# Kernel tuning notes

Measured on AMD Instinct MI355X. Metric: run time of the kernel, lower is better.

Reference implementation:

```python
import jax, jax.numpy as jnp
import numpy as np

OBS, ACT, EMB, DET, STO = 512, 32, 1024, 1024, 256
T, B = 64, 256
KL_SCALE = 1.0


def setup_inputs() -> dict:
    key = jax.random.key(0)
    ks = jax.random.split(key, 24)
    s = 0.02
    inp = {
        "obs": jax.random.normal(ks[0], (T, B, OBS), jnp.float32),
        "actions": jax.random.normal(ks[1], (T, B, ACT), jnp.float32),
        "rewards": jax.random.normal(ks[2], (T, B), jnp.float32),
        "dones": jnp.zeros((T, B), jnp.bool_),
        "eps": jax.random.normal(ks[3], (T - 1, B, STO), jnp.float32),
        # encoder: Linear(OBS,EMB) -> ReLU -> Linear(EMB,EMB) -> ReLU
        "enc_w1": jax.random.normal(ks[4], (OBS, EMB)) * s,
        "enc_b1": jnp.zeros((EMB,)),
        "enc_w2": jax.random.normal(ks[5], (EMB, EMB)) * s,
        "enc_b2": jnp.zeros((EMB,)),
        # GRUCell(STO+ACT, DET), torch layout [3*DET, in], gate order r,z,n
        "gru_wih": jax.random.normal(ks[6], (3 * DET, STO + ACT)) * s,
        "gru_whh": jax.random.normal(ks[7], (3 * DET, DET)) * s,
        "gru_bih": jnp.zeros((3 * DET,)),
        "gru_bhh": jnp.zeros((3 * DET,)),
        # prior / posterior nets
        "prior_w": jax.random.normal(ks[8], (DET, 2 * STO)) * s,
        "prior_b": jnp.zeros((2 * STO,)),
        "post_w": jax.random.normal(ks[9], (DET + EMB, 2 * STO)) * s,
        "post_b": jnp.zeros((2 * STO,)),
        # obs decoder
        "dec_w1": jax.random.normal(ks[10], (DET + STO, EMB)) * s,
        "dec_b1": jnp.zeros((EMB,)),
        "dec_w2": jax.random.normal(ks[11], (EMB, OBS)) * s,
        "dec_b2": jnp.zeros((OBS,)),
        # reward head
        "rew_w1": jax.random.normal(ks[12], (DET + STO, EMB)) * s,
        "rew_b1": jnp.zeros((EMB,)),
        "rew_w2": jax.random.normal(ks[13], (EMB, 1)) * s,
        "rew_b2": jnp.zeros((1,)),
    }
    return inp


def _kl(mq, lq, mp, lp):
    vq = jnp.exp(2.0 * lq)
    vp = jnp.exp(2.0 * lp)
    kl = lp - lq + (vq + (mq - mp) ** 2) / (vp + 1e-8) - 1.0
    return 0.5 * jnp.sum(kl, axis=-1)


def reference(obs, actions, rewards, dones, eps,
              enc_w1, enc_b1, enc_w2, enc_b2,
              gru_wih, gru_whh, gru_bih, gru_bhh,
              prior_w, prior_b, post_w, post_b,
              dec_w1, dec_b1, dec_w2, dec_b2,
              rew_w1, rew_b1, rew_w2, rew_b2):
    def step(carry, xs):
        h, z = carry
        o_t, o_next, a_t, r_t, d_t, e_t = xs
        # encoder
        emb = jax.nn.relu(jax.nn.relu(o_t @ enc_w1 + enc_b1) @ enc_w2 + enc_b2)
        # prior / posterior
        pm, pl = jnp.split(h @ prior_w + prior_b, 2, axis=-1)
        qm, ql = jnp.split(jnp.concatenate([h, emb], -1) @ post_w + post_b, 2, axis=-1)
        z_post = qm + e_t * jnp.exp(ql)
        # GRUCell (torch semantics)
        x = jnp.concatenate([z_post, a_t], -1)
        gi = x @ gru_wih.T + gru_bih
        gh = h @ gru_whh.T + gru_bhh
        ir, iz, inn = jnp.split(gi, 3, -1)
        hr, hz, hn = jnp.split(gh, 3, -1)
        r = jax.nn.sigmoid(ir + hr)
        u = jax.nn.sigmoid(iz + hz)
        n = jnp.tanh(inn + r * hn)
        h_next = (1.0 - u) * n + u * h
        feat = jnp.concatenate([h_next, z_post], -1)
        pred_obs = jax.nn.relu(feat @ dec_w1 + dec_b1) @ dec_w2 + dec_b2
        pred_rew = (jax.nn.relu(feat @ rew_w1 + rew_b1) @ rew_w2 + rew_b2)[..., 0]
        recon = jnp.mean((pred_obs - o_next) ** 2, axis=-1)  # [B]
        rew_l = (pred_rew - r_t) ** 2                         # [B]
        kl = _kl(qm, ql, pm, pl)                              # [B]
        mask = 1.0 - d_t.astype(h_next.dtype)[:, None]
        return (h_next * mask, z_post * mask), (recon, rew_l, kl)

    h0 = jnp.zeros((B, DET), obs.dtype)
    z0 = jnp.zeros((B, STO), obs.dtype)
    xs = (obs[:-1], obs[1:], actions[:-1], rewards[:-1], dones[:-1], eps)
    _, (recon, rew_l, kl) = jax.lax.scan(step, (h0, z0), xs)
    recon_loss = jnp.mean(recon)
    reward_loss = jnp.mean(rew_l)
    kl_loss = jnp.mean(kl)
    total = recon_loss + reward_loss + KL_SCALE * kl_loss
    return jnp.stack([total, recon_loss, reward_loss, kl_loss])
```

## Files before the change

### kernel.cpp

```cpp
#include <hip/hip_runtime.h>
#include <math.h>


namespace {

typedef unsigned short ushort;
typedef __attribute__((ext_vector_type(8))) short short8;
typedef __attribute__((ext_vector_type(4))) float f32x4;

constexpr int TSTEPS = 63;
constexpr int NB     = 256;
constexpr int NACT   = 32;
constexpr int NROWS  = TSTEPS * NB;
constexpr int TGRP   = 7;
constexpr int NGRP   = 9;
constexpr int GROWS  = TGRP * NB;

constexpr size_t OFF_POSTE = 0;
constexpr size_t OFF_OBSB  = OFF_POSTE + (size_t)NROWS * 512;
constexpr size_t OFF_E1C   = OFF_OBSB + (size_t)GROWS * 512 / 2;
constexpr size_t OFF_EMBC  = OFF_E1C + (size_t)GROWS * 1024 / 2;
constexpr size_t OFF_FEATC = OFF_EMBC + (size_t)GROWS * 1024 / 2;
constexpr size_t OFF_DR1C  = OFF_FEATC + (size_t)GROWS * 1280 / 2;
constexpr size_t OFF_WHT   = OFF_DR1C + (size_t)GROWS * 2048 / 2;
constexpr size_t OFF_WIHT  = OFF_WHT + (size_t)4096 * 1024 / 2;
constexpr size_t OFF_WDRT  = OFF_WIHT + (size_t)3072 * 288 / 2;
constexpr size_t OFF_E1T   = OFF_WDRT + (size_t)2048 * 1280 / 2;
constexpr size_t OFF_E2T   = OFF_E1T + (size_t)1024 * 512 / 2;
constexpr size_t OFF_PET   = OFF_E2T + (size_t)1024 * 1024 / 2;
constexpr size_t OFF_DW2T  = OFF_PET + (size_t)512 * 1024 / 2;
constexpr size_t OFF_BDR   = OFF_DW2T + (size_t)512 * 1024 / 2;
constexpr size_t OFF_G     = OFF_BDR + 2048;
constexpr size_t OFF_H     = OFF_G + (size_t)NB * 3072;
constexpr size_t OFF_HB    = OFF_H + (size_t)NB * 1024;
constexpr size_t OFF_ACC   = OFF_HB + (size_t)NB * 1024 / 2;
constexpr size_t OFF_XBUF  = OFF_ACC + 16;

__device__ __forceinline__ ushort f2bf(float f) {
  unsigned int u = __float_as_uint(f);
  unsigned int r = (u + 0x7fffu + ((u >> 16) & 1u)) >> 16;
  return (ushort)r;
}
__device__ __forceinline__ float bf2f(ushort u) {
  return __uint_as_float((unsigned int)u << 16);
}

__global__ void zero_kernel(float* p, int n) {
  int i = blockIdx.x * 256 + threadIdx.x;
  if (i < n) p[i] = 0.f;
}

__global__ void f2bf_kernel(const float* __restrict__ in, ushort* __restrict__ out, int n) {
  int i = blockIdx.x * 256 + threadIdx.x;
  if (i < n) out[i] = f2bf(in[i]);
}

__global__ void build_wht(const float* __restrict__ prior_w, const float* __restrict__ post_w,
                          const float* __restrict__ whh, ushort* __restrict__ out) {
  int idx = blockIdx.x * 256 + threadIdx.x;
  int n = idx >> 10, k = idx & 1023;
  float v;
  if (n < 1024) {
    int q = (n >> 4) & 3;
    int s = ((n >> 6) << 4) | (n & 15);
    v = (q == 0) ? prior_w[k * 512 + s]
      : (q == 1) ? prior_w[k * 512 + 256 + s]
      : (q == 2) ? post_w[k * 512 + s]
                 : post_w[k * 512 + 256 + s];
  } else {
    v = whh[(size_t)(n - 1024) * 1024 + k];
  }
  out[idx] = f2bf(v);
}

__global__ void trans_conv(const float* __restrict__ in, ushort* __restrict__ out,
                           int ldi, int ldo) {
  __shared__ float tile[32][33];
  int r0 = blockIdx.y * 32, c0 = blockIdx.x * 32;
  int tx = threadIdx.x & 31, ty = threadIdx.x >> 5;
#pragma unroll
  for (int p = 0; p < 4; ++p)
    tile[ty + p * 8][tx] = in[(size_t)(r0 + ty + p * 8) * ldi + c0 + tx];
  __syncthreads();
#pragma unroll
  for (int p = 0; p < 4; ++p)
    out[(size_t)(c0 + ty + p * 8) * ldo + r0 + tx] = f2bf(tile[tx][ty + p * 8]);
}

__global__ void build_bdr(const float* __restrict__ dec_b1, const float* __restrict__ rew_b1,
                          float* __restrict__ bdr) {
  int i = blockIdx.x * 256 + threadIdx.x;
  bdr[i] = (i < 1024) ? dec_b1[i] : rew_b1[i - 1024];
}

template <int EPI>
__global__ __launch_bounds__(256) void gemm_bf16(
    const ushort* __restrict__ A, const ushort* __restrict__ BT,
    const float* __restrict__ bias, void* __restrict__ Cv,
    int K, int lda, int ldb, int ldc) {
  __shared__ __align__(16) ushort As[64 * 40];
  __shared__ __align__(16) ushort Bs[64 * 40];
  int tid = threadIdx.x;
  int wave = tid >> 6, lane = tid & 63;
  int quad = lane >> 4, l15 = lane & 15;
  int m0 = blockIdx.y * 64, n0 = blockIdx.x * 64;
  int sr = tid >> 2, sc = (tid & 3) * 8;
  f32x4 acc[4] = {};
  for (int k0 = 0; k0 < K; k0 += 32) {
    *(int4*)&As[sr * 40 + sc] = *(const int4*)(A + (size_t)(m0 + sr) * lda + k0 + sc);
    *(int4*)&Bs[sr * 40 + sc] = *(const int4*)(BT + (size_t)(n0 + sr) * ldb + k0 + sc);
    __syncthreads();
    short8 a = *(const short8*)&As[(wave * 16 + l15) * 40 + quad * 8];
#pragma unroll
    for (int c = 0; c < 4; ++c) {
      short8 b = *(const short8*)&Bs[(c * 16 + l15) * 40 + quad * 8];
      acc[c] = __builtin_amdgcn_mfma_f32_16x16x32_bf16(a, b, acc[c], 0, 0, 0);
    }
    __syncthreads();
  }
#pragma unroll
  for (int c = 0; c < 4; ++c) {
#pragma unroll
    for (int r = 0; r < 4; ++r) {
      size_t row = m0 + wave * 16 + quad * 4 + r;
      int col = n0 + c * 16 + l15;
      float v = acc[c][r] + bias[col];
      if (EPI == 1) v = fmaxf(v, 0.f);
      if (EPI == 1) ((ushort*)Cv)[row * ldc + col] = f2bf(v);
      else ((float*)Cv)[row * ldc + col] = v;
    }
  }
}

__global__ __launch_bounds__(256) void step_g_kernel(
    int t, int tt, const ushort* __restrict__ HB, const ushort* __restrict__ WHT,
    const float* __restrict__ prior_b, const float* __restrict__ poste,
    const float* __restrict__ eps, const float* __restrict__ actions,
    float* __restrict__ G, ushort* __restrict__ xbuf,
    ushort* __restrict__ featc, float* __restrict__ acc_kl) {
  __shared__ __align__(16) ushort As[64 * 72];
  __shared__ __align__(16) ushort Bs[64 * 72];
  int tid = threadIdx.x;
  int wave = tid >> 6, lane = tid & 63;
  int quad = lane >> 4, l15 = lane & 15;
  int m0 = blockIdx.y * 64, n0 = blockIdx.x * 64;
  int sr = tid >> 2, sc = (tid & 3) * 16;
  const ushort* agp = HB + (size_t)(m0 + sr) * 1024 + sc;
  const ushort* bgp = WHT + (size_t)(n0 + sr) * 1024 + sc;
  int4 a0 = *(const int4*)agp, a1 = *(const int4*)(agp + 8);
  int4 b0 = *(const int4*)bgp, b1 = *(const int4*)(bgp + 8);
  f32x4 acc[4] = {};
  for (int k0 = 0;;) {
    *(int4*)&As[sr * 72 + sc] = a0; *(int4*)&As[sr * 72 + sc + 8] = a1;
    *(int4*)&Bs[sr * 72 + sc] = b0; *(int4*)&Bs[sr * 72 + sc + 8] = b1;
    __syncthreads();
    int kn = k0 + 64;
    if (kn < 1024) {
      a0 = *(const int4*)(agp + kn); a1 = *(const int4*)(agp + kn + 8);
      b0 = *(const int4*)(bgp + kn); b1 = *(const int4*)(bgp + kn + 8);
    }
#pragma unroll
    for (int kk = 0; kk < 2; ++kk) {
      short8 a = *(const short8*)&As[(wave * 16 + l15) * 72 + kk * 32 + quad * 8];
#pragma unroll
      for (int c = 0; c < 4; ++c) {
        short8 b = *(const short8*)&Bs[(c * 16 + l15) * 72 + kk * 32 + quad * 8];
        acc[c] = __builtin_amdgcn_mfma_f32_16x16x32_bf16(a, b, acc[c], 0, 0, 0);
      }
    }
    k0 = kn;
    if (k0 >= 1024) break;
    __syncthreads();
  }
  if (blockIdx.x < 16) {
    int s = (n0 >> 2) + l15;
    float kl_sum = 0.f;
#pragma unroll
    for (int r = 0; r < 4; ++r) {
      int b = m0 + wave * 16 + quad * 4 + r;
      size_t row = (size_t)t * NB + b;
      float pm = acc[0][r] + prior_b[s];
      float pl = acc[1][r] + prior_b[256 + s];
      float qm = acc[2][r] + poste[row * 512 + s];
      float ql = acc[3][r] + poste[row * 512 + 256 + s];
      float e = eps[row * 256 + s];
      float z = qm + e * expf(ql);
      xbuf[b * 288 + s] = f2bf(z);
      featc[(size_t)(tt * NB + b) * 1280 + 1024 + s] = f2bf(z);
      if (s < NACT) xbuf[b * 288 + 256 + s] = f2bf(actions[row * NACT + s]);
      float vq = expf(2.f * ql), vp = expf(2.f * pl);
      float dm = qm - pm;
      kl_sum += pl - ql + (vq + dm * dm) / (vp + 1e-8f) - 1.f;
    }
    for (int off = 32; off > 0; off >>= 1) kl_sum += __shfl_down(kl_sum, off);
    if (lane == 0) atomicAdd(acc_kl, 0.5f * kl_sum);
  } else {
    int ng = n0 - 1024;
#pragma unroll
    for (int c = 0; c < 4; ++c)
#pragma unroll
      for (int r = 0; r < 4; ++r) {
        int b = m0 + wave * 16 + quad * 4 + r;
        G[(size_t)b * 3072 + ng + c * 16 + l15] = acc[c][r];
      }
  }
}

__global__ __launch_bounds__(256) void gru_step_kernel(
    int t, int tt, const ushort* __restrict__ xbuf, const ushort* __restrict__ wiht,
    const float* __restrict__ G, const float* __restrict__ bih,
    const float* __restrict__ bhh, const unsigned char* __restrict__ dones,
    float* __restrict__ H, ushort* __restrict__ HB, ushort* __restrict__ featc) {
  __shared__ __align__(16) ushort As[64 * 40];
  __shared__ __align__(16) ushort Bs[3][64 * 40];
  int tid = threadIdx.x;
  int wave = tid >> 6, lane = tid & 63;
  int quad = lane >> 4, l15 = lane & 15;
  int m0 = blockIdx.y * 64, n0 = blockIdx.x * 64;
  int sr = tid >> 2, sc = (tid & 3) * 8;
  const ushort* agp = xbuf + (size_t)(m0 + sr) * 288 + sc;
  const ushort* bgp0 = wiht + (size_t)(n0 + sr) * 288 + sc;
  int4 pa = *(const int4*)agp;
  int4 pb0 = *(const int4*)bgp0;
  int4 pb1 = *(const int4*)(bgp0 + (size_t)1024 * 288);
  int4 pb2 = *(const int4*)(bgp0 + (size_t)2048 * 288);
  f32x4 accv[3][4] = {};
  for (int k0 = 0;;) {
    *(int4*)&As[sr * 40 + sc] = pa;
    *(int4*)&Bs[0][sr * 40 + sc] = pb0;
    *(int4*)&Bs[1][sr * 40 + sc] = pb1;
    *(int4*)&Bs[2][sr * 40 + sc] = pb2;
    __syncthreads();
    int kn = k0 + 32;
    if (kn < 288) {
      pa = *(const int4*)(agp + kn);
      pb0 = *(const int4*)(bgp0 + kn);
      pb1 = *(const int4*)(bgp0 + (size_t)1024 * 288 + kn);
      pb2 = *(const int4*)(bgp0 + (size_t)2048 * 288 + kn);
    }
    short8 a = *(const short8*)&As[(wave * 16 + l15) * 40 + quad * 8];
#pragma unroll
    for (int gg = 0; gg < 3; ++gg) {
#pragma unroll
      for (int c = 0; c < 4; ++c) {
        short8 b = *(const short8*)&Bs[gg][(c * 16 + l15) * 40 + quad * 8];
        accv[gg][c] = __builtin_amdgcn_mfma_f32_16x16x32_bf16(a, b, accv[gg][c], 0, 0, 0);
      }
    }
    k0 = kn;
    if (k0 >= 288) break;
    __syncthreads();
  }
#pragma unroll
  for (int c = 0; c < 4; ++c) {
#pragma unroll
    for (int r = 0; r < 4; ++r) {
      int b_idx = m0 + wave * 16 + quad * 4 + r;
      int j = n0 + c * 16 + l15;
      const float* g = G + (size_t)b_idx * 3072;
      float ir = accv[0][c][r] + bih[j];
      float iz = accv[1][c][r] + bih[1024 + j];
      float in_ = accv[2][c][r] + bih[2048 + j];
      float hr = g[j] + bhh[j];
      float hz = g[1024 + j] + bhh[1024 + j];
      float hn = g[2048 + j] + bhh[2048 + j];
      float rg = 1.f / (1.f + expf(-(ir + hr)));
      float u = 1.f / (1.f + expf(-(iz + hz)));
      float n = tanhf(in_ + rg * hn);
      float hprev = H[b_idx * 1024 + j];
      float hnext = (1.f - u) * n + u * hprev;
      featc[(size_t)(tt * NB + b_idx) * 1280 + j] = f2bf(hnext);
      float mask = 1.f - (float)dones[t * NB + b_idx];
      float hm = hnext * mask;
      H[b_idx * 1024 + j] = hm;
      HB[b_idx * 1024 + j] = f2bf(hm);
    }
  }
}

__global__ __launch_bounds__(256) void decobs_loss_kernel(
    const ushort* __restrict__ A, const ushort* __restrict__ BT,
    const float* __restrict__ bias, const float* __restrict__ obs_next_g,
    float* __restrict__ acc) {
  __shared__ __align__(16) ushort As[64 * 40];
  __shared__ __align__(16) ushort Bs[64 * 40];
  int tid = threadIdx.x;
  int wave = tid >> 6, lane = tid & 63;
  int quad = lane >> 4, l15 = lane & 15;
  int m0 = blockIdx.y * 64, n0 = blockIdx.x * 64;
  int sr = tid >> 2, sc = (tid & 3) * 8;
  f32x4 accm[4] = {};
  for (int k0 = 0; k0 < 1024; k0 += 32) {
    *(int4*)&As[sr * 40 + sc] = *(const int4*)(A + (size_t)(m0 + sr) * 2048 + k0 + sc);
    *(int4*)&Bs[sr * 40 + sc] = *(const int4*)(BT + (size_t)(n0 + sr) * 1024 + k0 + sc);
    __syncthreads();
    short8 a = *(const short8*)&As[(wave * 16 + l15) * 40 + quad * 8];
#pragma unroll
    for (int c = 0; c < 4; ++c) {
      short8 b = *(const short8*)&Bs[(c * 16 + l15) * 40 + quad * 8];
      accm[c] = __builtin_amdgcn_mfma_f32_16x16x32_bf16(a, b, accm[c], 0, 0, 0);
    }
    __syncthreads();
  }
  float local = 0.f;
#pragma unroll
  for (int c = 0; c < 4; ++c) {
#pragma unroll
    for (int r = 0; r < 4; ++r) {
      size_t row = m0 + wave * 16 + quad * 4 + r;
      int col = n0 + c * 16 + l15;
      float v = accm[c][r] + bias[col];
      float d = v - obs_next_g[row * 512 + col];
      local += d * d;
    }
  }
  __shared__ float red[256];
  red[tid] = local;
  __syncthreads();
  for (int st = 128; st > 0; st >>= 1) {
    if (tid < st) red[tid] += red[tid + st];
    __syncthreads();
  }
  if (tid == 0) atomicAdd(&acc[0], red[0]);
}

__global__ __launch_bounds__(256) void rew_loss_kernel(
    const ushort* __restrict__ R1, const float* __restrict__ w2,
    const float* __restrict__ b2, const float* __restrict__ rewards_g,
    float* __restrict__ acc) {
  int wave = threadIdx.x >> 6;
  int lane = threadIdx.x & 63;
  int row = blockIdx.x * 4 + wave;
  const ushort* rp = R1 + (size_t)row * 2048;
  float s = 0.f;
#pragma unroll
  for (int i = 0; i < 16; ++i) s += bf2f(rp[lane + 64 * i]) * w2[lane + 64 * i];
  for (int off = 32; off > 0; off >>= 1) s += __shfl_down(s, off);
  if (lane == 0) {
    float d = s + b2[0] - rewards_g[row];
    atomicAdd(&acc[1], d * d);
  }
}

__global__ void finalize_kernel(const float* __restrict__ acc, float* __restrict__ out) {
  float recon = acc[0] / ((float)NROWS * 512.f);
  float rew = acc[1] / (float)NROWS;
  float kl = acc[2] / (float)NROWS;
  out[0] = recon + rew + kl;
  out[1] = recon;
  out[2] = rew;
  out[3] = kl;
}

}

extern "C" void kernel_launch(void* const* d_in, const int* in_sizes, int n_in,
                              void* d_out, int out_size, void* d_ws, size_t ws_size,
                              hipStream_t stream) {
  const float* obs     = (const float*)d_in[0];
  const float* actions = (const float*)d_in[1];
  const float* rewards = (const float*)d_in[2];
  const unsigned char* dones = (const unsigned char*)d_in[3];
  const float* eps     = (const float*)d_in[4];
  const float* enc_w1  = (const float*)d_in[5];
  const float* enc_b1  = (const float*)d_in[6];
  const float* enc_w2  = (const float*)d_in[7];
  const float* enc_b2  = (const float*)d_in[8];
  const float* gru_wih = (const float*)d_in[9];
  const float* gru_whh = (const float*)d_in[10];
  const float* gru_bih = (const float*)d_in[11];
  const float* gru_bhh = (const float*)d_in[12];
  const float* prior_w = (const float*)d_in[13];
  const float* prior_b = (const float*)d_in[14];
  const float* post_w  = (const float*)d_in[15];
  const float* post_b  = (const float*)d_in[16];
  const float* dec_w1  = (const float*)d_in[17];
  const float* dec_b1  = (const float*)d_in[18];
  const float* dec_w2  = (const float*)d_in[19];
  const float* dec_b2  = (const float*)d_in[20];
  const float* rew_w1  = (const float*)d_in[21];
  const float* rew_b1  = (const float*)d_in[22];
  const float* rew_w2  = (const float*)d_in[23];
  const float* rew_b2  = (const float*)d_in[24];
  float* out = (float*)d_out;
  float* ws = (float*)d_ws;

  float*  POSTE = ws + OFF_POSTE;
  ushort* OBSB  = (ushort*)(ws + OFF_OBSB);
  ushort* E1C   = (ushort*)(ws + OFF_E1C);
  ushort* EMBC  = (ushort*)(ws + OFF_EMBC);
  ushort* FEATC = (ushort*)(ws + OFF_FEATC);
  ushort* DR1C  = (ushort*)(ws + OFF_DR1C);
  ushort* WHT   = (ushort*)(ws + OFF_WHT);
  ushort* WIHT  = (ushort*)(ws + OFF_WIHT);
  ushort* WDRT  = (ushort*)(ws + OFF_WDRT);
  ushort* E1T   = (ushort*)(ws + OFF_E1T);
  ushort* E2T   = (ushort*)(ws + OFF_E2T);
  ushort* PET   = (ushort*)(ws + OFF_PET);
  ushort* DW2T  = (ushort*)(ws + OFF_DW2T);
  float*  BDR   = ws + OFF_BDR;
  float*  G     = ws + OFF_G;
  float*  H     = ws + OFF_H;
  ushort* HB    = (ushort*)(ws + OFF_HB);
  float*  ACC   = ws + OFF_ACC;
  ushort* XBUF  = (ushort*)(ws + OFF_XBUF);

  {
    int nzero = NB * 1024 + NB * 512 + 16;
    zero_kernel<<<(nzero + 255) / 256, 256, 0, stream>>>(H, nzero);
  }
  build_wht<<<4096 * 1024 / 256, 256, 0, stream>>>(prior_w, post_w, gru_whh, WHT);
  f2bf_kernel<<<(3072 * 288) / 256, 256, 0, stream>>>(gru_wih, WIHT, 3072 * 288);
  trans_conv<<<dim3(1024 / 32, 1280 / 32), 256, 0, stream>>>(dec_w1, WDRT, 1024, 1280);
  trans_conv<<<dim3(1024 / 32, 1280 / 32), 256, 0, stream>>>(rew_w1, WDRT + (size_t)1024 * 1280, 1024, 1280);
  trans_conv<<<dim3(1024 / 32, 512 / 32), 256, 0, stream>>>(enc_w1, E1T, 1024, 512);
  trans_conv<<<dim3(1024 / 32, 1024 / 32), 256, 0, stream>>>(enc_w2, E2T, 1024, 1024);
  trans_conv<<<dim3(512 / 32, 1024 / 32), 256, 0, stream>>>(post_w + (size_t)1024 * 512, PET, 512, 1024);
  trans_conv<<<dim3(512 / 32, 1024 / 32), 256, 0, stream>>>(dec_w2, DW2T, 512, 1024);
  build_bdr<<<8, 256, 0, stream>>>(dec_b1, rew_b1, BDR);

  for (int g = 0; g < NGRP; ++g) {
    const float* obs_g = obs + (size_t)g * GROWS * 512;
    f2bf_kernel<<<(GROWS * 512) / 256, 256, 0, stream>>>(obs_g, OBSB, GROWS * 512);
    gemm_bf16<1><<<dim3(16, GROWS / 64), 256, 0, stream>>>(
        OBSB, E1T, enc_b1, E1C, 512, 512, 512, 1024);
    gemm_bf16<1><<<dim3(16, GROWS / 64), 256, 0, stream>>>(
        E1C, E2T, enc_b2, EMBC, 1024, 1024, 1024, 1024);
    gemm_bf16<2><<<dim3(8, GROWS / 64), 256, 0, stream>>>(
        EMBC, PET, post_b, POSTE + (size_t)g * GROWS * 512, 1024, 1024, 1024, 512);
  }

  for (int g = 0; g < NGRP; ++g) {
    for (int tt = 0; tt < TGRP; ++tt) {
      int t = g * TGRP + tt;
      step_g_kernel<<<dim3(64, 4), 256, 0, stream>>>(
          t, tt, HB, WHT, prior_b, POSTE, eps, actions, G, XBUF, FEATC, &ACC[2]);
      gru_step_kernel<<<dim3(16, 4), 256, 0, stream>>>(
          t, tt, XBUF, WIHT, G, gru_bih, gru_bhh, dones, H, HB, FEATC);
    }
    gemm_bf16<1><<<dim3(32, GROWS / 64), 256, 0, stream>>>(
        FEATC, WDRT, BDR, DR1C, 1280, 1280, 1280, 2048);
    decobs_loss_kernel<<<dim3(8, GROWS / 64), 256, 0, stream>>>(
        DR1C, DW2T, dec_b2, obs + ((size_t)g * TGRP + 1) * NB * 512, ACC);
    rew_loss_kernel<<<GROWS / 4, 256, 0, stream>>>(
        DR1C + 1024, rew_w2, rew_b2, rewards + (size_t)g * TGRP * NB, ACC);
  }

  finalize_kernel<<<1, 1, 0, stream>>>(ACC, out);
}
```

Measured before the change: 3.129 ms.

## Double-buffer LDS in GEMM kernels, fuse obs conversion, split GRU step blocks

All GEMM-style kernels now use double-buffered shared memory with register prefetch of the next K tile. This removes the second barrier per K iteration and overlaps global loads with MFMA work. The encoder's first GEMM reads the fp32 observations directly and converts them to bf16 in registers, which drops the separate f2bf pass and its intermediate buffer. The GRU step kernel switches to 128-thread blocks covering 32 rows each, doubling the number of blocks for the small recurrent step. The cost is twice the LDS per block.

Result: faster. 3.044 ms (-2.7%).

```diff
diff --git a/kernel.cpp b/kernel.cpp
--- a/kernel.cpp
+++ b/kernel.cpp
@@ -93,30 +93,54 @@
   bdr[i] = (i < 1024) ? dec_b1[i] : rew_b1[i - 1024];
 }
 
-template <int EPI>
+template <int EPI, bool AF32>
 __global__ __launch_bounds__(256) void gemm_bf16(
-    const ushort* __restrict__ A, const ushort* __restrict__ BT,
+    const void* __restrict__ Av, const ushort* __restrict__ BT,
     const float* __restrict__ bias, void* __restrict__ Cv,
     int K, int lda, int ldb, int ldc) {
-  __shared__ __align__(16) ushort As[64 * 40];
-  __shared__ __align__(16) ushort Bs[64 * 40];
+  __shared__ __align__(16) ushort As[2][64 * 40];
+  __shared__ __align__(16) ushort Bs[2][64 * 40];
   int tid = threadIdx.x;
   int wave = tid >> 6, lane = tid & 63;
   int quad = lane >> 4, l15 = lane & 15;
   int m0 = blockIdx.y * 64, n0 = blockIdx.x * 64;
   int sr = tid >> 2, sc = (tid & 3) * 8;
+  const ushort* agb = (const ushort*)Av + (size_t)(m0 + sr) * lda + sc;
+  const float*  agf = (const float*)Av + (size_t)(m0 + sr) * lda + sc;
+  const ushort* bgp = BT + (size_t)(n0 + sr) * ldb + sc;
+  int4 pa0, pa1, pb;
+  if (AF32) { pa0 = *(const int4*)agf; pa1 = *(const int4*)(agf + 4); }
+  else      { pa0 = *(const int4*)agb; }
+  pb = *(const int4*)bgp;
   f32x4 acc[4] = {};
-  for (int k0 = 0; k0 < K; k0 += 32) {
-    *(int4*)&As[sr * 40 + sc] = *(const int4*)(A + (size_t)(m0 + sr) * lda + k0 + sc);
-    *(int4*)&Bs[sr * 40 + sc] = *(const int4*)(BT + (size_t)(n0 + sr) * ldb + k0 + sc);
+  int buf = 0;
+  for (int k0 = 0; k0 < K; k0 += 32, buf ^= 1) {
+    int4 st;
+    if (AF32) {
+      float f[8];
+      *(int4*)&f[0] = pa0; *(int4*)&f[4] = pa1;
+      ushort u[8];
+#pragma unroll
+      for (int i = 0; i < 8; ++i) u[i] = f2bf(f[i]);
+      st = *(const int4*)u;
+    } else {
+      st = pa0;
+    }
+    *(int4*)&As[buf][sr * 40 + sc] = st;
+    *(int4*)&Bs[buf][sr * 40 + sc] = pb;
     __syncthreads();
-    short8 a = *(const short8*)&As[(wave * 16 + l15) * 40 + quad * 8];
+    int kn = k0 + 32;
+    if (kn < K) {
+      if (AF32) { pa0 = *(const int4*)(agf + kn); pa1 = *(const int4*)(agf + kn + 4); }
+      else      { pa0 = *(const int4*)(agb + kn); }
+      pb = *(const int4*)(bgp + kn);
+    }
+    short8 a = *(const short8*)&As[buf][(wave * 16 + l15) * 40 + quad * 8];
 #pragma unroll
     for (int c = 0; c < 4; ++c) {
-      short8 b = *(const short8*)&Bs[(c * 16 + l15) * 40 + quad * 8];
+      short8 b = *(const short8*)&Bs[buf][(c * 16 + l15) * 40 + quad * 8];
       acc[c] = __builtin_amdgcn_mfma_f32_16x16x32_bf16(a, b, acc[c], 0, 0, 0);
     }
-    __syncthreads();
   }
 #pragma unroll
   for (int c = 0; c < 4; ++c) {
@@ -138,8 +162,8 @@
     const float* __restrict__ eps, const float* __restrict__ actions,
     float* __restrict__ G, ushort* __restrict__ xbuf,
     ushort* __restrict__ featc, float* __restrict__ acc_kl) {
-  __shared__ __align__(16) ushort As[64 * 72];
-  __shared__ __align__(16) ushort Bs[64 * 72];
+  __shared__ __align__(16) ushort As[2][64 * 72];
+  __shared__ __align__(16) ushort Bs[2][64 * 72];
   int tid = threadIdx.x;
   int wave = tid >> 6, lane = tid & 63;
   int quad = lane >> 4, l15 = lane & 15;
@@ -150,9 +174,10 @@
   int4 a0 = *(const int4*)agp, a1 = *(const int4*)(agp + 8);
   int4 b0 = *(const int4*)bgp, b1 = *(const int4*)(bgp + 8);
   f32x4 acc[4] = {};
-  for (int k0 = 0;;) {
-    *(int4*)&As[sr * 72 + sc] = a0; *(int4*)&As[sr * 72 + sc + 8] = a1;
-    *(int4*)&Bs[sr * 72 + sc] = b0; *(int4*)&Bs[sr * 72 + sc + 8] = b1;
+  int buf = 0;
+  for (int k0 = 0; k0 < 1024; k0 += 64, buf ^= 1) {
+    *(int4*)&As[buf][sr * 72 + sc] = a0; *(int4*)&As[buf][sr * 72 + sc + 8] = a1;
+    *(int4*)&Bs[buf][sr * 72 + sc] = b0; *(int4*)&Bs[buf][sr * 72 + sc + 8] = b1;
     __syncthreads();
     int kn = k0 + 64;
     if (kn < 1024) {
@@ -161,16 +186,13 @@
     }
 #pragma unroll
     for (int kk = 0; kk < 2; ++kk) {
-      short8 a = *(const short8*)&As[(wave * 16 + l15) * 72 + kk * 32 + quad * 8];
+      short8 a = *(const short8*)&As[buf][(wave * 16 + l15) * 72 + kk * 32 + quad * 8];
 #pragma unroll
       for (int c = 0; c < 4; ++c) {
-        short8 b = *(const short8*)&Bs[(c * 16 + l15) * 72 + kk * 32 + quad * 8];
+        short8 b = *(const short8*)&Bs[buf][(c * 16 + l15) * 72 + kk * 32 + quad * 8];
         acc[c] = __builtin_amdgcn_mfma_f32_16x16x32_bf16(a, b, acc[c], 0, 0, 0);
       }
     }
-    k0 = kn;
-    if (k0 >= 1024) break;
-    __syncthreads();
   }
   if (blockIdx.x < 16) {
     int s = (n0 >> 2) + l15;
@@ -206,50 +228,56 @@
   }
 }
 
-__global__ __launch_bounds__(256) void gru_step_kernel(
+__global__ __launch_bounds__(128) void gru_step_kernel(
     int t, int tt, const ushort* __restrict__ xbuf, const ushort* __restrict__ wiht,
     const float* __restrict__ G, const float* __restrict__ bih,
     const float* __restrict__ bhh, const unsigned char* __restrict__ dones,
     float* __restrict__ H, ushort* __restrict__ HB, ushort* __restrict__ featc) {
-  __shared__ __align__(16) ushort As[64 * 40];
-  __shared__ __align__(16) ushort Bs[3][64 * 40];
+  __shared__ __align__(16) ushort As[2][32 * 40];
+  __shared__ __align__(16) ushort Bs[2][3][64 * 40];
   int tid = threadIdx.x;
   int wave = tid >> 6, lane = tid & 63;
   int quad = lane >> 4, l15 = lane & 15;
-  int m0 = blockIdx.y * 64, n0 = blockIdx.x * 64;
-  int sr = tid >> 2, sc = (tid & 3) * 8;
-  const ushort* agp = xbuf + (size_t)(m0 + sr) * 288 + sc;
-  const ushort* bgp0 = wiht + (size_t)(n0 + sr) * 288 + sc;
+  int m0 = blockIdx.y * 32, n0 = blockIdx.x * 64;
+  int ar = tid >> 2, ac = (tid & 3) * 8;
+  int br = tid >> 1, bc = (tid & 1) * 16;
+  const ushort* agp = xbuf + (size_t)(m0 + ar) * 288 + ac;
+  const ushort* bgp = wiht + (size_t)(n0 + br) * 288 + bc;
   int4 pa = *(const int4*)agp;
-  int4 pb0 = *(const int4*)bgp0;
-  int4 pb1 = *(const int4*)(bgp0 + (size_t)1024 * 288);
-  int4 pb2 = *(const int4*)(bgp0 + (size_t)2048 * 288);
+  int4 pb[3][2];
+#pragma unroll
+  for (int gg = 0; gg < 3; ++gg) {
+    pb[gg][0] = *(const int4*)(bgp + (size_t)gg * 1024 * 288);
+    pb[gg][1] = *(const int4*)(bgp + (size_t)gg * 1024 * 288 + 8);
+  }
   f32x4 accv[3][4] = {};
-  for (int k0 = 0;;) {
-    *(int4*)&As[sr * 40 + sc] = pa;
-    *(int4*)&Bs[0][sr * 40 + sc] = pb0;
-    *(int4*)&Bs[1][sr * 40 + sc] = pb1;
-    *(int4*)&Bs[2][sr * 40 + sc] = pb2;
+  int buf = 0;
+  for (int k0 = 0; k0 < 288; k0 += 32, buf ^= 1) {
+    *(int4*)&As[buf][ar * 40 + ac] = pa;
+#pragma unroll
+    for (int gg = 0; gg < 3; ++gg) {
+      *(int4*)&Bs[buf][gg][br * 40 + bc] = pb[gg][0];
+      *(int4*)&Bs[buf][gg][br * 40 + bc + 8] = pb[gg][1];
+    }
     __syncthreads();
     int kn = k0 + 32;
     if (kn < 288) {
       pa = *(const int4*)(agp + kn);
-      pb0 = *(const int4*)(bgp0 + kn);
-      pb1 = *(const int4*)(bgp0 + (size_t)1024 * 288 + kn);
-      pb2 = *(const int4*)(bgp0 + (size_t)2048 * 288 + kn);
-    }
-    short8 a = *(const short8*)&As[(wave * 16 + l15) * 40 + quad * 8];
+#pragma unroll
+      for (int gg = 0; gg < 3; ++gg) {
+        pb[gg][0] = *(const int4*)(bgp + (size_t)gg * 1024 * 288 + kn);
+        pb[gg][1] = *(const int4*)(bgp + (size_t)gg * 1024 * 288 + kn + 8);
+      }
+    }
+    short8 a = *(const short8*)&As[buf][(wave * 16 + l15) * 40 + quad * 8];
 #pragma unroll
     for (int gg = 0; gg < 3; ++gg) {
 #pragma unroll
       for (int c = 0; c < 4; ++c) {
-        short8 b = *(const short8*)&Bs[gg][(c * 16 + l15) * 40 + quad * 8];
+        short8 b = *(const short8*)&Bs[buf][gg][(c * 16 + l15) * 40 + quad * 8];
         accv[gg][c] = __builtin_amdgcn_mfma_f32_16x16x32_bf16(a, b, accv[gg][c], 0, 0, 0);
       }
     }
-    k0 = kn;
-    if (k0 >= 288) break;
-    __syncthreads();
   }
 #pragma unroll
   for (int c = 0; c < 4; ++c) {
@@ -282,25 +310,34 @@
     const ushort* __restrict__ A, const ushort* __restrict__ BT,
     const float* __restrict__ bias, const float* __restrict__ obs_next_g,
     float* __restrict__ acc) {
-  __shared__ __align__(16) ushort As[64 * 40];
-  __shared__ __align__(16) ushort Bs[64 * 40];
+  __shared__ __align__(16) ushort As[2][64 * 40];
+  __shared__ __align__(16) ushort Bs[2][64 * 40];
   int tid = threadIdx.x;
   int wave = tid >> 6, lane = tid & 63;
   int quad = lane >> 4, l15 = lane & 15;
   int m0 = blockIdx.y * 64, n0 = blockIdx.x * 64;
   int sr = tid >> 2, sc = (tid & 3) * 8;
+  const ushort* agp = A + (size_t)(m0 + sr) * 2048 + sc;
+  const ushort* bgp = BT + (size_t)(n0 + sr) * 1024 + sc;
+  int4 pa = *(const int4*)agp;
+  int4 pb = *(const int4*)bgp;
   f32x4 accm[4] = {};
-  for (int k0 = 0; k0 < 1024; k0 += 32) {
-    *(int4*)&As[sr * 40 + sc] = *(const int4*)(A + (size_t)(m0 + sr) * 2048 + k0 + sc);
-    *(int4*)&Bs[sr * 40 + sc] = *(const int4*)(BT + (size_t)(n0 + sr) * 1024 + k0 + sc);
+  int buf = 0;
+  for (int k0 = 0; k0 < 1024; k0 += 32, buf ^= 1) {
+    *(int4*)&As[buf][sr * 40 + sc] = pa;
+    *(int4*)&Bs[buf][sr * 40 + sc] = pb;
     __syncthreads();
-    short8 a = *(const short8*)&As[(wave * 16 + l15) * 40 + quad * 8];
+    int kn = k0 + 32;
+    if (kn < 1024) {
+      pa = *(const int4*)(agp + kn);
+      pb = *(const int4*)(bgp + kn);
+    }
+    short8 a = *(const short8*)&As[buf][(wave * 16 + l15) * 40 + quad * 8];
 #pragma unroll
     for (int c = 0; c < 4; ++c) {
-      short8 b = *(const short8*)&Bs[(c * 16 + l15) * 40 + quad * 8];
+      short8 b = *(const short8*)&Bs[buf][(c * 16 + l15) * 40 + quad * 8];
       accm[c] = __builtin_amdgcn_mfma_f32_16x16x32_bf16(a, b, accm[c], 0, 0, 0);
     }
-    __syncthreads();
   }
   float local = 0.f;
 #pragma unroll
@@ -386,7 +423,6 @@
   float* ws = (float*)d_ws;
 
   float*  POSTE = ws + OFF_POSTE;
-  ushort* OBSB  = (ushort*)(ws + OFF_OBSB);
   ushort* E1C   = (ushort*)(ws + OFF_E1C);
   ushort* EMBC  = (ushort*)(ws + OFF_EMBC);
   ushort* FEATC = (ushort*)(ws + OFF_FEATC);
@@ -421,13 +457,12 @@
 
   for (int g = 0; g < NGRP; ++g) {
     const float* obs_g = obs + (size_t)g * GROWS * 512;
-    f2bf_kernel<<<(GROWS * 512) / 256, 256, 0, stream>>>(obs_g, OBSB, GROWS * 512);
-    gemm_bf16<1><<<dim3(16, GROWS / 64), 256, 0, stream>>>(
-        OBSB, E1T, enc_b1, E1C, 512, 512, 512, 1024);
-    gemm_bf16<1><<<dim3(16, GROWS / 64), 256, 0, stream>>>(
-        E1C, E2T, enc_b2, EMBC, 1024, 1024, 1024, 1024);
-    gemm_bf16<2><<<dim3(8, GROWS / 64), 256, 0, stream>>>(
-        EMBC, PET, post_b, POSTE + (size_t)g * GROWS * 512, 1024, 1024, 1024, 512);
+    gemm_bf16<1, true><<<dim3(16, GROWS / 64), 256, 0, stream>>>(
+        (const void*)obs_g, E1T, enc_b1, E1C, 512, 512, 512, 1024);
+    gemm_bf16<1, false><<<dim3(16, GROWS / 64), 256, 0, stream>>>(
+        (const void*)E1C, E2T, enc_b2, EMBC, 1024, 1024, 1024, 1024);
+    gemm_bf16<2, false><<<dim3(8, GROWS / 64), 256, 0, stream>>>(
+        (const void*)EMBC, PET, post_b, POSTE + (size_t)g * GROWS * 512, 1024, 1024, 1024, 512);
   }
 
   for (int g = 0; g < NGRP; ++g) {
@@ -435,11 +470,11 @@
       int t = g * TGRP + tt;
       step_g_kernel<<<dim3(64, 4), 256, 0, stream>>>(
           t, tt, HB, WHT, prior_b, POSTE, eps, actions, G, XBUF, FEATC, &ACC[2]);
-      gru_step_kernel<<<dim3(16, 4), 256, 0, stream>>>(
+      gru_step_kernel<<<dim3(16, 8), 128, 0, stream>>>(
           t, tt, XBUF, WIHT, G, gru_bih, gru_bhh, dones, H, HB, FEATC);
     }
-    gemm_bf16<1><<<dim3(32, GROWS / 64), 256, 0, stream>>>(
-        FEATC, WDRT, BDR, DR1C, 1280, 1280, 1280, 2048);
+    gemm_bf16<1, false><<<dim3(32, GROWS / 64), 256, 0, stream>>>(
+        (const void*)FEATC, WDRT, BDR, DR1C, 1280, 1280, 1280, 2048);
     decobs_loss_kernel<<<dim3(8, GROWS / 64), 256, 0, stream>>>(
         DR1C, DW2T, dec_b2, obs + ((size_t)g * TGRP + 1) * NB * 512, ACC);
     rew_loss_kernel<<<GROWS / 4, 256, 0, stream>>>(
```
